# Kernel tuning notes

Hardware: AMD Instinct MI355X
Metric: run time of the kernel (lower is better)

## Reference

```python
import jax, jax.numpy as jnp
import numpy as np

B, C, S, E, H = 16, 24, 128, 256, 8
P = E // H  # head projection dim (consistent interpretation of the buggy source)
EPS = 1e-6


def _ln(x, g, b):
    mu = jnp.mean(x, axis=-1, keepdims=True)
    var = jnp.mean((x - mu) ** 2, axis=-1, keepdims=True)
    return (x - mu) * jax.lax.rsqrt(var + EPS) * g + b


def setup_inputs() -> dict:
    key = jax.random.key(0)
    ks = jax.random.split(key, 16)
    s = 0.02
    return {
        'x': jax.random.normal(ks[0], (B, C, S, E), jnp.float32),
        # spatial attention params
        'Wq_s': s * jax.random.normal(ks[1], (H, C, P, E), jnp.float32),
        'Wk_s': s * jax.random.normal(ks[2], (H, E, P), jnp.float32),
        'Wv_s': s * jax.random.normal(ks[3], (H, E, P), jnp.float32),
        'Wo_s': s * jax.random.normal(ks[4], (C, E, E), jnp.float32),
        # temporal attention params
        'Wq_t': s * jax.random.normal(ks[5], (H, C, E, P), jnp.float32),
        'Wk_t': s * jax.random.normal(ks[6], (H, C, E, P), jnp.float32),
        'Wv_t': s * jax.random.normal(ks[7], (H, C, E, P), jnp.float32),
        'Wo_t': s * jax.random.normal(ks[8], (C, E, E), jnp.float32),
        # shared layernorm
        'ln_g': jnp.ones((E,), jnp.float32),
        'ln_b': jnp.zeros((E,), jnp.float32),
        # per-joint pointwise FF (Linear->ReLU->Linear)
        'ff_w1': s * jax.random.normal(ks[9], (C, E, E), jnp.float32),
        'ff_b1': jnp.zeros((C, E), jnp.float32),
        'ff_w2': s * jax.random.normal(ks[10], (C, E, E), jnp.float32),
        'ff_b2': jnp.zeros((C, E), jnp.float32),
    }


def _spatial_attention(x, Wq, Wk, Wv, Wo):
    # x: [B,C,S,E]; per-head per-joint query proj, shared key/value proj
    q = jnp.einsum('bcse,hcpe->bshcp', x, Wq)          # [B,S,H,C,P]
    k = jnp.einsum('bcse,hep->bshcp', x, Wk)
    v = jnp.einsum('bcse,hep->bshcp', x, Wv)
    scores = jnp.einsum('bshcp,bshdp->bshcd', q, k) / jnp.sqrt(jnp.float32(P))
    a = jax.nn.softmax(scores, axis=-1)                # attn over joints d
    o = jnp.einsum('bshcd,bshdp->bshcp', a, v)
    o = o.transpose(0, 3, 1, 2, 4).reshape(x.shape[0], C, x.shape[2], H * P)  # [B,C,S,E]
    return jnp.einsum('bcse,cef->bcsf', o, Wo)


def _temporal_attention(x, Wq, Wk, Wv, Wo):
    q = jnp.einsum('bcse,hcep->bhcsp', x, Wq)          # [B,H,C,S,P]
    k = jnp.einsum('bcse,hcep->bhcsp', x, Wk)
    v = jnp.einsum('bcse,hcep->bhcsp', x, Wv)
    scores = jnp.einsum('bhcsp,bhctp->bhcst', q, k) / jnp.sqrt(jnp.float32(P))
    a = jax.nn.softmax(scores, axis=-1)                # attn over time t
    o = jnp.einsum('bhcst,bhctp->bhcsp', a, v)
    o = o.transpose(0, 2, 3, 1, 4).reshape(x.shape[0], C, x.shape[2], H * P)  # [B,C,S,E]
    return jnp.einsum('bcse,cef->bcsf', o, Wo)


def reference(x, Wq_s, Wk_s, Wv_s, Wo_s, Wq_t, Wk_t, Wv_t, Wo_t, ln_g, ln_b, ff_w1, ff_b1, ff_w2, ff_b2):
    spat = _spatial_attention(x, Wq_s, Wk_s, Wv_s, Wo_s)
    temp = _temporal_attention(x, Wq_t, Wk_t, Wv_t, Wo_t)
    attn_out = _ln(x + spat, ln_g, ln_b) + _ln(x + temp, ln_g, ln_b)
    # per-joint pointwise FF, vectorized over joints
    h = jax.nn.relu(jnp.einsum('bcse,cef->bcsf', attn_out, ff_w1) + ff_b1[None, :, None, :])
    ff = jnp.einsum('bcse,cef->bcsf', h, ff_w2) + ff_b2[None, :, None, :]
    return _ln(attn_out + ff, ln_g, ln_b)
```

## Files before the change

### kernel.cpp

```cpp
#include <hip/hip_runtime.h>
#include <hip/hip_bf16.h>

constexpr int Bn = 16, Cn = 24, Sn = 128, En = 256, Hn = 8, Pn = 32;
constexpr int NROWS = Bn * Cn * Sn;
constexpr size_t NBUF = (size_t)Bn * Cn * Sn * En;
constexpr size_t WSLOT = (size_t)Cn * 256 * 256;

typedef __bf16 bf16_t;
typedef bf16_t bf16x8 __attribute__((ext_vector_type(8)));
typedef bf16_t bf16x4 __attribute__((ext_vector_type(4)));
typedef float f32x4 __attribute__((ext_vector_type(4)));

__device__ __forceinline__ void gl2lds16(const bf16_t* g, bf16_t* l) {
    typedef const __attribute__((address_space(1))) unsigned int* gp_t;
    typedef __attribute__((address_space(3))) unsigned int* lp_t;
    __builtin_amdgcn_global_load_lds((gp_t)(unsigned long long)g,
                                     (lp_t)(unsigned int)(unsigned long long)l,
                                     16, 0, 0);
}

__global__ __launch_bounds__(256) void conv_x_k(const float* __restrict__ x,
                                                bf16_t* __restrict__ xb) {
    const size_t i = ((size_t)blockIdx.x * 256 + threadIdx.x) * 4;
    const float4 v = *(const float4*)(x + i);
    bf16x4 o = {(bf16_t)v.x, (bf16_t)v.y, (bf16_t)v.z, (bf16_t)v.w};
    *(bf16x4*)(xb + i) = o;
}

__global__ __launch_bounds__(256) void conv_w_copy_k(const float* __restrict__ W,
                                                     bf16_t* __restrict__ out) {
    const int row = blockIdx.x * 4 + (threadIdx.x >> 6);
    const int lane = threadIdx.x & 63;
    const int n = row & 255, c = row >> 8;
    const float* src = W + (size_t)c * (Pn * En) + (size_t)(n >> 5) * (Cn * Pn * En) +
                       (size_t)(n & 31) * En + lane * 4;
    const float4 v = *(const float4*)src;
    bf16x4 o = {(bf16_t)v.x, (bf16_t)v.y, (bf16_t)v.z, (bf16_t)v.w};
    *(bf16x4*)(out + (size_t)row * 256 + lane * 4) = o;
}

struct TDesc { const float* W; int Sc, Snh, Se; };

__global__ __launch_bounds__(256) void conv_w_tr_k(
    TDesc d0, TDesc d1, TDesc d2, TDesc d3, TDesc d4, TDesc d5, TDesc d6,
    bf16_t* __restrict__ out)
{
    TDesc d;
    switch (blockIdx.z) {
        case 0: d = d0; break; case 1: d = d1; break; case 2: d = d2; break;
        case 3: d = d3; break; case 4: d = d4; break; case 5: d = d5; break;
        default: d = d6; break;
    }
    const int g = blockIdx.x & 7, et = blockIdx.x >> 3;
    const int c = blockIdx.y;

    __shared__ float tile[32][65];

    const int t = threadIdx.x;
    const float* base = d.W + (size_t)c * d.Sc + (size_t)g * d.Snh;

#pragma unroll
    for (int pass = 0; pass < 2; ++pass) {
        const int e_local = pass * 32 + (t >> 3);
        const int j4 = (t & 7) * 4;
        const float4 v = *(const float4*)(base + (size_t)(et * 64 + e_local) * d.Se + j4);
        tile[j4 + 0][e_local] = v.x;
        tile[j4 + 1][e_local] = v.y;
        tile[j4 + 2][e_local] = v.z;
        tile[j4 + 3][e_local] = v.w;
    }
    __syncthreads();

    const int j = t >> 3, e8 = (t & 7) * 8;
    bf16x8 o;
#pragma unroll
    for (int k = 0; k < 8; ++k) o[k] = (bf16_t)tile[j][e8 + k];
    *(bf16x8*)(out + (size_t)blockIdx.z * WSLOT +
               ((size_t)c * 256 + g * 32 + j) * 256 + et * 64 + e8) = o;
}

__global__ __launch_bounds__(256) void conv_w_k(const float* __restrict__ W,
                                                bf16_t* __restrict__ Wb,
                                                int Sc, int Snh, int Snp, int Se) {
    const int n = blockIdx.x & 255, c = blockIdx.x >> 8;
    const int e = threadIdx.x;
    Wb[(size_t)blockIdx.x * 256 + e] =
        (bf16_t)W[(size_t)c * Sc + (size_t)(n >> 5) * Snh + (n & 31) * Snp + (size_t)e * Se];
}

struct GDesc { const bf16_t* W; bf16_t* O; int Aoff, Wc, Ob, Oc, Os, Onh, Onp, trans; };

template <int NP, int EPI>
__global__ __launch_bounds__(256) void gemm_mfma(
    const bf16_t* __restrict__ A, int Ab, int Ac, int As,
    GDesc g0, GDesc g1, GDesc g2, const float* __restrict__ bias)
{
    const int b = blockIdx.x, c = blockIdx.z;
    const int proj = (NP == 1) ? 0 : ((int)blockIdx.y >> 1);
    const int nt = (NP == 1) ? (int)blockIdx.y : ((int)blockIdx.y & 1);
    GDesc g = (proj == 0) ? g0 : (proj == 1) ? g1 : g2;

    __shared__ bf16_t smem[3][2][128 * 32];
    bf16_t* Cs = &smem[0][0][0];

    const int tid = threadIdx.x, wv = tid >> 6, ln = tid & 63;
    const int wm = (wv >> 1) * 64, wn = (wv & 1) * 64;
    const int lr = ln & 15, hi = ln >> 4, lk = hi * 8;

    const bf16_t* Abase = A + g.Aoff + (size_t)b * Ab + (size_t)c * Ac;
    const bf16_t* Bbase = g.W + (size_t)c * g.Wc + (size_t)(nt * 128) * 256;

    auto stage = [&](int buf, int kt) {
        const int k0 = kt * 32;
#pragma unroll
        for (int it = 0; it < 2; ++it) {
            const int cb = it * 256 + wv * 64;
            const int mc = cb + ln;
            const int row = mc >> 2, kc = (mc & 3) * 8;
            gl2lds16(Abase + (size_t)row * As + k0 + kc, &smem[buf][0][cb * 8]);
            gl2lds16(Bbase + (size_t)row * 256 + k0 + kc, &smem[buf][1][cb * 8]);
        }
    };

    f32x4 acc[4][4] = {};

    stage(0, 0);
    stage(1, 1);

#pragma unroll
    for (int kt = 0; kt < 8; ++kt) {
        if (kt < 6) stage((kt + 2) % 3, kt + 2);
        if (kt < 6)       asm volatile("s_waitcnt vmcnt(8)" ::: "memory");
        else if (kt == 6) asm volatile("s_waitcnt vmcnt(4)" ::: "memory");
        else              asm volatile("s_waitcnt vmcnt(0)" ::: "memory");
        __builtin_amdgcn_s_barrier();
        __builtin_amdgcn_sched_barrier(0);

        const int cur = kt % 3;
        bf16x8 af[4], bfr[4];
#pragma unroll
        for (int i = 0; i < 4; ++i)
            af[i] = *(const bf16x8*)&smem[cur][0][(wm + i * 16 + lr) * 32 + lk];
#pragma unroll
        for (int j = 0; j < 4; ++j)
            bfr[j] = *(const bf16x8*)&smem[cur][1][(wn + j * 16 + lr) * 32 + lk];
        __builtin_amdgcn_s_setprio(1);
#pragma unroll
        for (int i = 0; i < 4; ++i)
#pragma unroll
            for (int j = 0; j < 4; ++j)
                acc[i][j] = __builtin_amdgcn_mfma_f32_16x16x32_bf16(af[i], bfr[j], acc[i][j], 0, 0, 0);
        __builtin_amdgcn_s_setprio(0);

        __builtin_amdgcn_sched_barrier(0);
        __builtin_amdgcn_s_barrier();
    }

#pragma unroll
    for (int pass = 0; pass < 2; ++pass) {
        if (!g.trans) {
            if (wm == pass * 64) {
#pragma unroll
                for (int i = 0; i < 4; ++i)
#pragma unroll
                    for (int j = 0; j < 4; ++j) {
                        const int n = nt * 128 + wn + j * 16 + lr;
                        float bv = 0.f;
                        if (EPI) bv = bias[c * 256 + n];
#pragma unroll
                        for (int r = 0; r < 4; ++r) {
                            float v = acc[i][j][r];
                            if (EPI) { v += bv; if (EPI == 1) v = fmaxf(v, 0.f); }
                            Cs[(i * 16 + hi * 4 + r) * 136 + wn + j * 16 + lr] = (bf16_t)v;
                        }
                    }
            }
            __syncthreads();
#pragma unroll
            for (int it = 0; it < 2; ++it) {
                const int lrow = it * 32 + (tid >> 3);
                const int n0 = (tid & 7) * 16;
                bf16x8 v0 = *(const bf16x8*)&Cs[lrow * 136 + n0];
                bf16x8 v1 = *(const bf16x8*)&Cs[lrow * 136 + n0 + 8];
                const int m = pass * 64 + lrow;
                const int n = nt * 128 + n0;
                bf16_t* dst = g.O + (size_t)b * g.Ob + (size_t)c * g.Oc +
                              (size_t)m * g.Os + (size_t)(n >> 5) * g.Onh + (n & 31);
                *(bf16x8*)dst = v0;
                *(bf16x8*)(dst + 8) = v1;
            }
            __syncthreads();
        } else {
            if (wn == pass * 64) {
#pragma unroll
                for (int i = 0; i < 4; ++i)
#pragma unroll
                    for (int j = 0; j < 4; ++j) {
                        bf16x4 pk = {(bf16_t)acc[i][j][0], (bf16_t)acc[i][j][1],
                                     (bf16_t)acc[i][j][2], (bf16_t)acc[i][j][3]};
                        *(bf16x4*)&Cs[(j * 16 + lr) * 136 + wm + i * 16 + hi * 4] = pk;
                    }
            }
            __syncthreads();
#pragma unroll
            for (int it = 0; it < 2; ++it) {
                const int lrow = it * 32 + (tid >> 3);
                const int m0 = (tid & 7) * 16;
                bf16x8 v0 = *(const bf16x8*)&Cs[lrow * 136 + m0];
                bf16x8 v1 = *(const bf16x8*)&Cs[lrow * 136 + m0 + 8];
                const int n = nt * 128 + pass * 64 + lrow;
                bf16_t* dst = g.O + (size_t)b * g.Ob + (size_t)c * g.Oc +
                              (size_t)(n >> 5) * g.Onh + (size_t)(n & 31) * g.Onp + m0;
                *(bf16x8*)dst = v0;
                *(bf16x8*)(dst + 8) = v1;
            }
            __syncthreads();
        }
    }
}

__global__ __launch_bounds__(256) void attn_spatial_mfma(
    const bf16_t* __restrict__ Q, const bf16_t* __restrict__ K,
    const bf16_t* __restrict__ V, bf16_t* __restrict__ O)
{
    __shared__ bf16_t Ps[4][32 * 40];
    __shared__ bf16_t Vt[4][32 * 40];

    const int tid = threadIdx.x, wv = tid >> 6, ln = tid & 63;
    const int lr = ln & 15, hi = ln >> 4, lk = hi * 8;

    const int bsh = blockIdx.x * 4 + wv;
    const int h = bsh & 7, s = (bsh >> 3) & 127, b = bsh >> 10;
    const size_t qb = (size_t)bsh * (Cn * Pn);

    {
        const int p = ln >> 1, c0 = 24 + (ln & 1) * 4;
        bf16x4 z = {};
        *(bf16x4*)&Vt[wv][p * 40 + c0] = z;
    }
#pragma unroll
    for (int it = 0; it < 2; ++it) {
        const int ch = it * 64 + ln;
        if (ch < 96) {
            const int cc = ch >> 2, p0 = (ch & 3) * 8;
            bf16x8 v = *(const bf16x8*)(V + qb + cc * 32 + p0);
#pragma unroll
            for (int j = 0; j < 8; ++j)
                Vt[wv][(p0 + j) * 40 + cc] = v[j];
        }
    }

    bf16x8 aq0 = *(const bf16x8*)(Q + qb + lr * 32 + lk);
    bf16x8 aq1 = *(const bf16x8*)(Q + qb + (16 + lr) * 32 + lk);
    bf16x8 bk0 = *(const bf16x8*)(K + qb + lr * 32 + lk);
    bf16x8 bk1 = *(const bf16x8*)(K + qb + (16 + lr) * 32 + lk);
    const f32x4 zz = {0.f, 0.f, 0.f, 0.f};
    f32x4 sc[2][2];
    sc[0][0] = __builtin_amdgcn_mfma_f32_16x16x32_bf16(aq0, bk0, zz, 0, 0, 0);
    sc[0][1] = __builtin_amdgcn_mfma_f32_16x16x32_bf16(aq0, bk1, zz, 0, 0, 0);
    sc[1][0] = __builtin_amdgcn_mfma_f32_16x16x32_bf16(aq1, bk0, zz, 0, 0, 0);
    sc[1][1] = __builtin_amdgcn_mfma_f32_16x16x32_bf16(aq1, bk1, zz, 0, 0, 0);

    const float scale = 0.17677669529663687f;
#pragma unroll
    for (int i = 0; i < 2; ++i) {
        float s0[4], s1[4], mx[4];
#pragma unroll
        for (int r = 0; r < 4; ++r) {
            s0[r] = sc[i][0][r] * scale;
            s1[r] = (lr >= 8) ? -3.0e38f : sc[i][1][r] * scale;
            mx[r] = fmaxf(s0[r], s1[r]);
        }
#pragma unroll
        for (int d = 1; d < 16; d <<= 1)
#pragma unroll
            for (int r = 0; r < 4; ++r) mx[r] = fmaxf(mx[r], __shfl_xor(mx[r], d));
        float e0[4], e1[4], sm[4];
#pragma unroll
        for (int r = 0; r < 4; ++r) {
            e0[r] = __expf(s0[r] - mx[r]);
            e1[r] = __expf(s1[r] - mx[r]);
            sm[r] = e0[r] + e1[r];
        }
#pragma unroll
        for (int d = 1; d < 16; d <<= 1)
#pragma unroll
            for (int r = 0; r < 4; ++r) sm[r] += __shfl_xor(sm[r], d);
#pragma unroll
        for (int r = 0; r < 4; ++r) {
            const float inv = 1.f / sm[r];
            const int row = i * 16 + hi * 4 + r;
            Ps[wv][row * 40 + lr]      = (bf16_t)(e0[r] * inv);
            Ps[wv][row * 40 + 16 + lr] = (bf16_t)(e1[r] * inv);
        }
    }

    bf16x8 ap0 = *(const bf16x8*)&Ps[wv][lr * 40 + lk];
    bf16x8 ap1 = *(const bf16x8*)&Ps[wv][(16 + lr) * 40 + lk];
    bf16x8 bv0 = *(const bf16x8*)&Vt[wv][lr * 40 + lk];
    bf16x8 bv1 = *(const bf16x8*)&Vt[wv][(16 + lr) * 40 + lk];
    f32x4 o[2][2];
    o[0][0] = __builtin_amdgcn_mfma_f32_16x16x32_bf16(ap0, bv0, zz, 0, 0, 0);
    o[0][1] = __builtin_amdgcn_mfma_f32_16x16x32_bf16(ap0, bv1, zz, 0, 0, 0);
    o[1][0] = __builtin_amdgcn_mfma_f32_16x16x32_bf16(ap1, bv0, zz, 0, 0, 0);
    o[1][1] = __builtin_amdgcn_mfma_f32_16x16x32_bf16(ap1, bv1, zz, 0, 0, 0);

#pragma unroll
    for (int i = 0; i < 2; ++i)
#pragma unroll
        for (int r = 0; r < 4; ++r) {
            const int c = i * 16 + hi * 4 + r;
            if (c < 24) {
                const size_t ob = ((size_t)(b * Cn + c) * Sn + s) * En + h * Pn;
#pragma unroll
                for (int j = 0; j < 2; ++j)
                    O[ob + j * 16 + lr] = (bf16_t)o[i][j][r];
            }
        }
}

__global__ __launch_bounds__(256) void attn_temporal_mfma(
    const bf16_t* __restrict__ Q, const bf16_t* __restrict__ K,
    const bf16_t* __restrict__ Vt, bf16_t* __restrict__ O)
{
    const int c = blockIdx.x, h = blockIdx.y, b = blockIdx.z;
    const size_t base = ((size_t)(b * Hn + h) * Cn + c) * (Sn * Pn);

    __shared__ bf16_t Qs[128 * 32];
    __shared__ bf16_t Ks[128 * 32];
    __shared__ bf16_t Vs[32 * 136];
    __shared__ bf16_t Ps[128 * 136];

    const int tid = threadIdx.x, wv = tid >> 6, ln = tid & 63;
    const int lr = ln & 15, lk = (ln >> 4) * 8;

#pragma unroll
    for (int it = 0; it < 2; ++it) {
        const int cb = it * 256 + wv * 64;
        const int mc = cb + ln;
        const int row = mc >> 2, kc = (mc & 3) * 8;
        gl2lds16(Q + base + row * 32 + kc, &Qs[cb * 8]);
        gl2lds16(K + base + row * 32 + kc, &Ks[cb * 8]);
    }
#pragma unroll
    for (int it = 0; it < 2; ++it) {
        const int mc = it * 256 + tid;
        const int p = mc >> 4, scn = (mc & 15) * 8;
        bf16x8 v = *(const bf16x8*)(Vt + base + p * 128 + scn);
        *(bf16x8*)&Vs[p * 136 + scn] = v;
    }
    __syncthreads();

    const int r0 = wv * 32;
    bf16x8 aq0 = *(const bf16x8*)&Qs[(r0 + lr) * 32 + lk];
    bf16x8 aq1 = *(const bf16x8*)&Qs[(r0 + 16 + lr) * 32 + lk];
    f32x4 sc_[2][8];
    const f32x4 zz = {0.f, 0.f, 0.f, 0.f};
#pragma unroll
    for (int j = 0; j < 8; ++j) {
        bf16x8 bk = *(const bf16x8*)&Ks[(j * 16 + lr) * 32 + lk];
        sc_[0][j] = __builtin_amdgcn_mfma_f32_16x16x32_bf16(aq0, bk, zz, 0, 0, 0);
        sc_[1][j] = __builtin_amdgcn_mfma_f32_16x16x32_bf16(aq1, bk, zz, 0, 0, 0);
    }

    const float scale = 0.17677669529663687f;
#pragma unroll
    for (int i = 0; i < 2; ++i) {
        float mx[4], sm[4];
#pragma unroll
        for (int r = 0; r < 4; ++r) {
            float m = sc_[i][0][r];
#pragma unroll
            for (int j = 1; j < 8; ++j) m = fmaxf(m, sc_[i][j][r]);
            mx[r] = m;
        }
#pragma unroll
        for (int d = 1; d < 16; d <<= 1)
#pragma unroll
            for (int r = 0; r < 4; ++r) mx[r] = fmaxf(mx[r], __shfl_xor(mx[r], d));
#pragma unroll
        for (int r = 0; r < 4; ++r) sm[r] = 0.f;
#pragma unroll
        for (int j = 0; j < 8; ++j)
#pragma unroll
            for (int r = 0; r < 4; ++r) {
                const float e = __expf((sc_[i][j][r] - mx[r]) * scale);
                sc_[i][j][r] = e; sm[r] += e;
            }
#pragma unroll
        for (int d = 1; d < 16; d <<= 1)
#pragma unroll
            for (int r = 0; r < 4; ++r) sm[r] += __shfl_xor(sm[r], d);
        float inv[4];
#pragma unroll
        for (int r = 0; r < 4; ++r) inv[r] = 1.f / sm[r];
        const int rb = r0 + i * 16 + (ln >> 4) * 4;
#pragma unroll
        for (int j = 0; j < 8; ++j)
#pragma unroll
            for (int r = 0; r < 4; ++r)
                Ps[(rb + r) * 136 + j * 16 + lr] = (bf16_t)(sc_[i][j][r] * inv[r]);
    }
    __syncthreads();

    f32x4 o[2][2] = {};
#pragma unroll
    for (int kk = 0; kk < 4; ++kk) {
        bf16x8 ap0 = *(const bf16x8*)&Ps[(r0 + lr) * 136 + kk * 32 + lk];
        bf16x8 ap1 = *(const bf16x8*)&Ps[(r0 + 16 + lr) * 136 + kk * 32 + lk];
        bf16x8 bv0 = *(const bf16x8*)&Vs[lr * 136 + kk * 32 + lk];
        bf16x8 bv1 = *(const bf16x8*)&Vs[(16 + lr) * 136 + kk * 32 + lk];
        o[0][0] = __builtin_amdgcn_mfma_f32_16x16x32_bf16(ap0, bv0, o[0][0], 0, 0, 0);
        o[0][1] = __builtin_amdgcn_mfma_f32_16x16x32_bf16(ap0, bv1, o[0][1], 0, 0, 0);
        o[1][0] = __builtin_amdgcn_mfma_f32_16x16x32_bf16(ap1, bv0, o[1][0], 0, 0, 0);
        o[1][1] = __builtin_amdgcn_mfma_f32_16x16x32_bf16(ap1, bv1, o[1][1], 0, 0, 0);
    }

#pragma unroll
    for (int i = 0; i < 2; ++i) {
        const int sb = r0 + i * 16 + (ln >> 4) * 4;
#pragma unroll
        for (int j = 0; j < 2; ++j) {
            const int p = h * 32 + j * 16 + lr;
#pragma unroll
            for (int r = 0; r < 4; ++r)
                O[((size_t)(b * Cn + c) * Sn + (sb + r)) * En + p] = (bf16_t)o[i][j][r];
        }
    }
}

__global__ __launch_bounds__(256) void ln_combine_k(
    const bf16_t* __restrict__ xb, const bf16_t* __restrict__ spat,
    const bf16_t* __restrict__ temp, const float* __restrict__ g,
    const float* __restrict__ beta, bf16_t* __restrict__ AO)
{
    const int row = blockIdx.x * 4 + (threadIdx.x >> 6);
    const int lane = threadIdx.x & 63;
    const size_t off = (size_t)row * En;

    float v1[4], v2[4];
    float s1 = 0, s2 = 0, q1 = 0, q2 = 0;
#pragma unroll
    for (int i = 0; i < 4; i++) {
        const int e = lane + i * 64;
        const float xv = (float)xb[off + e];
        const float a = xv + (float)spat[off + e];
        const float t = xv + (float)temp[off + e];
        v1[i] = a; v2[i] = t;
        s1 += a; s2 += t; q1 += a * a; q2 += t * t;
    }
    for (int d = 32; d; d >>= 1) {
        s1 += __shfl_xor(s1, d); s2 += __shfl_xor(s2, d);
        q1 += __shfl_xor(q1, d); q2 += __shfl_xor(q2, d);
    }
    const float mu1 = s1 / En, mu2 = s2 / En;
    const float r1 = rsqrtf(q1 / En - mu1 * mu1 + 1e-6f);
    const float r2 = rsqrtf(q2 / En - mu2 * mu2 + 1e-6f);
#pragma unroll
    for (int i = 0; i < 4; i++) {
        const int e = lane + i * 64;
        const float out = (v1[i] - mu1) * r1 * g[e] + beta[e] +
                          (v2[i] - mu2) * r2 * g[e] + beta[e];
        AO[off + e] = (bf16_t)out;
    }
}

__global__ __launch_bounds__(256) void ln_final_k(
    const bf16_t* __restrict__ AO, const bf16_t* __restrict__ FF,
    const float* __restrict__ g, const float* __restrict__ beta,
    float* __restrict__ out)
{
    const int row = blockIdx.x * 4 + (threadIdx.x >> 6);
    const int lane = threadIdx.x & 63;
    const size_t off = (size_t)row * En;

    float v[4];
    float s = 0, q = 0;
#pragma unroll
    for (int i = 0; i < 4; i++) {
        const int e = lane + i * 64;
        const float a = (float)AO[off + e] + (float)FF[off + e];
        v[i] = a; s += a; q += a * a;
    }
    for (int d = 32; d; d >>= 1) { s += __shfl_xor(s, d); q += __shfl_xor(q, d); }
    const float mu = s / En;
    const float r = rsqrtf(q / En - mu * mu + 1e-6f);
#pragma unroll
    for (int i = 0; i < 4; i++) {
        const int e = lane + i * 64;
        out[off + e] = (v[i] - mu) * r * g[e] + beta[e];
    }
}

extern "C" void kernel_launch(void* const* d_in, const int* in_sizes, int n_in,
                              void* d_out, int out_size, void* d_ws, size_t ws_size,
                              hipStream_t stream)
{
    const float* x     = (const float*)d_in[0];
    const float* Wq_s  = (const float*)d_in[1];
    const float* Wk_s  = (const float*)d_in[2];
    const float* Wv_s  = (const float*)d_in[3];
    const float* Wo_s  = (const float*)d_in[4];
    const float* Wq_t  = (const float*)d_in[5];
    const float* Wk_t  = (const float*)d_in[6];
    const float* Wv_t  = (const float*)d_in[7];
    const float* Wo_t  = (const float*)d_in[8];
    const float* ln_g  = (const float*)d_in[9];
    const float* ln_b  = (const float*)d_in[10];
    const float* ff_w1 = (const float*)d_in[11];
    const float* ff_b1 = (const float*)d_in[12];
    const float* ff_w2 = (const float*)d_in[13];
    const float* ff_b2 = (const float*)d_in[14];
    float* out = (float*)d_out;

    bf16_t* wsb = (bf16_t*)d_ws;
    bf16_t* b0 = wsb;
    bf16_t* b1 = wsb + NBUF;
    bf16_t* b2 = wsb + 2 * NBUF;
    bf16_t* b3 = wsb + 3 * NBUF;
    bf16_t* b4 = wsb + 4 * NBUF;

    bf16_t* xb = (bf16_t*)d_out;
    bf16_t* wb = xb + NBUF;
    bf16_t* w_qs = wb + 0 * WSLOT;
    bf16_t* wtr  = wb + 1 * WSLOT;
    bf16_t* w_os = wtr + 0 * WSLOT;
    bf16_t* w_qt = wtr + 1 * WSLOT;
    bf16_t* w_kt = wtr + 2 * WSLOT;
    bf16_t* w_vt = wtr + 3 * WSLOT;
    bf16_t* w_ot = wtr + 4 * WSLOT;
    bf16_t* w_f1 = wtr + 5 * WSLOT;
    bf16_t* w_f2 = wtr + 6 * WSLOT;
    bf16_t* w_ks = b4 + NBUF - 2 * 65536;
    bf16_t* w_vs = b4 + NBUF - 65536;

    const int XAb = Cn * Sn * En, XAc = Sn * En, XAs = En;
    const int QSb = Sn * Hn * Cn * Pn, QSs = Hn * Cn * Pn, QSh = Cn * Pn;
    const int QTb = Hn * Cn * Sn * Pn, QTh = Cn * Sn * Pn, QTc = Sn * Pn, QTs = Pn;
    const int WCP = 256 * 256;

    conv_x_k<<<NBUF / 1024, 256, 0, stream>>>(x, xb);
    conv_w_copy_k<<<1536, 256, 0, stream>>>(Wq_s, w_qs);
    conv_w_tr_k<<<dim3(32, 24, 7), 256, 0, stream>>>(
        TDesc{Wo_s, En * En, Pn, En},
        TDesc{Wq_t, En * Pn, Cn * En * Pn, Pn},
        TDesc{Wk_t, En * Pn, Cn * En * Pn, Pn},
        TDesc{Wv_t, En * Pn, Cn * En * Pn, Pn},
        TDesc{Wo_t, En * En, Pn, En},
        TDesc{ff_w1, En * En, Pn, En},
        TDesc{ff_w2, En * En, Pn, En},
        wtr);
    conv_w_k<<<256, 256, 0, stream>>>(Wk_s, w_ks, 0, En * Pn, 1, Pn);
    conv_w_k<<<256, 256, 0, stream>>>(Wv_s, w_vs, 0, En * Pn, 1, Pn);

    gemm_mfma<3, 0><<<dim3(16, 6, 24), 256, 0, stream>>>(
        xb, XAb, XAc, XAs,
        GDesc{w_qs, b0, 0, WCP, QSb, Pn, QSs, QSh, 1, 0},
        GDesc{w_ks, b1, 0, 0,   QSb, Pn, QSs, QSh, 1, 0},
        GDesc{w_vs, b2, 0, 0,   QSb, Pn, QSs, QSh, 1, 0},
        nullptr);
    attn_spatial_mfma<<<Bn * Sn * Hn / 4, 256, 0, stream>>>(b0, b1, b2, b3);

    gemm_mfma<3, 0><<<dim3(16, 6, 24), 256, 0, stream>>>(
        xb, XAb, XAc, XAs,
        GDesc{w_qt, b0, 0, WCP, QTb, QTc, QTs, QTh, 1, 0},
        GDesc{w_kt, b1, 0, WCP, QTb, QTc, QTs, QTh, 1, 0},
        GDesc{w_vt, b2, 0, WCP, QTb, QTc, 1, QTh, Sn, 1},
        nullptr);
    attn_temporal_mfma<<<dim3(24, 8, 16), 256, 0, stream>>>(b0, b1, b2, b4);

    gemm_mfma<2, 0><<<dim3(16, 4, 24), 256, 0, stream>>>(
        b3, XAb, XAc, XAs,
        GDesc{w_os, b0, 0,          WCP, XAb, XAc, XAs, 32, 1, 0},
        GDesc{w_ot, b1, (int)NBUF,  WCP, XAb, XAc, XAs, 32, 1, 0},
        GDesc{w_os, b0, 0,          WCP, XAb, XAc, XAs, 32, 1, 0}, nullptr);

    ln_combine_k<<<NROWS / 4, 256, 0, stream>>>(xb, b0, b1, ln_g, ln_b, b2);
    gemm_mfma<1, 1><<<dim3(16, 2, 24), 256, 0, stream>>>(
        b2, XAb, XAc, XAs,
        GDesc{w_f1, b3, 0, WCP, XAb, XAc, XAs, 32, 1, 0},
        GDesc{w_f1, b3, 0, WCP, XAb, XAc, XAs, 32, 1, 0},
        GDesc{w_f1, b3, 0, WCP, XAb, XAc, XAs, 32, 1, 0}, ff_b1);
    gemm_mfma<1, 2><<<dim3(16, 2, 24), 256, 0, stream>>>(
        b3, XAb, XAc, XAs,
        GDesc{w_f2, b4, 0, WCP, XAb, XAc, XAs, 32, 1, 0},
        GDesc{w_f2, b4, 0, WCP, XAb, XAc, XAs, 32, 1, 0},
        GDesc{w_f2, b4, 0, WCP, XAb, XAc, XAs, 32, 1, 0}, ff_b2);
    ln_final_k<<<NROWS / 4, 256, 0, stream>>>(b2, b4, ln_g, ln_b, out);
}
```

Measured before the change: 387.8 us.

## Enlarge GEMM tile to 256x128 spanning two batches per block

```diff
diff --git a/kernel.cpp b/kernel.cpp
--- a/kernel.cpp
+++ b/kernel.cpp
@@ -91,38 +91,43 @@
 struct GDesc { const bf16_t* W; bf16_t* O; int Aoff, Wc, Ob, Oc, Os, Onh, Onp, trans; };
 
 template <int NP, int EPI>
-__global__ __launch_bounds__(256) void gemm_mfma(
+__global__ __launch_bounds__(256, 2) void gemm_mfma(
     const bf16_t* __restrict__ A, int Ab, int Ac, int As,
     GDesc g0, GDesc g1, GDesc g2, const float* __restrict__ bias)
 {
-    const int b = blockIdx.x, c = blockIdx.z;
+    const int bx = blockIdx.x, c = blockIdx.z;
     const int proj = (NP == 1) ? 0 : ((int)blockIdx.y >> 1);
     const int nt = (NP == 1) ? (int)blockIdx.y : ((int)blockIdx.y & 1);
     GDesc g = (proj == 0) ? g0 : (proj == 1) ? g1 : g2;
 
-    __shared__ bf16_t smem[3][2][128 * 32];
-    bf16_t* Cs = &smem[0][0][0];
+    __shared__ bf16_t smem[3][12288];
+    bf16_t* Cs = &smem[0][0];
 
     const int tid = threadIdx.x, wv = tid >> 6, ln = tid & 63;
-    const int wm = (wv >> 1) * 64, wn = (wv & 1) * 64;
+    const int wm = wv * 64;
     const int lr = ln & 15, hi = ln >> 4, lk = hi * 8;
 
-    const bf16_t* Abase = A + g.Aoff + (size_t)b * Ab + (size_t)c * Ac;
+    const bf16_t* Abase = A + g.Aoff + (size_t)(bx * 2) * Ab + (size_t)c * Ac;
     const bf16_t* Bbase = g.W + (size_t)c * g.Wc + (size_t)(nt * 128) * 256;
 
     auto stage = [&](int buf, int kt) {
         const int k0 = kt * 32;
 #pragma unroll
-        for (int it = 0; it < 2; ++it) {
-            const int cb = it * 256 + wv * 64;
-            const int mc = cb + ln;
-            const int row = mc >> 2, kc = (mc & 3) * 8;
-            gl2lds16(Abase + (size_t)row * As + k0 + kc, &smem[buf][0][cb * 8]);
-            gl2lds16(Bbase + (size_t)row * 256 + k0 + kc, &smem[buf][1][cb * 8]);
+        for (int ga = 0; ga < 4; ++ga) {
+            const int ch = ga * 256 + wv * 64 + ln;
+            const int row = ch >> 2, q = (ch & 3) * 8;
+            gl2lds16(Abase + (size_t)(row >> 7) * Ab + (size_t)(row & 127) * As + k0 + q,
+                     &smem[buf][ch * 8]);
+        }
+#pragma unroll
+        for (int gb = 0; gb < 2; ++gb) {
+            const int ch = gb * 256 + wv * 64 + ln;
+            const int row = ch >> 2, q = (ch & 3) * 8;
+            gl2lds16(Bbase + (size_t)row * 256 + k0 + q, &smem[buf][8192 + ch * 8]);
         }
     };
 
-    f32x4 acc[4][4] = {};
+    f32x4 acc[4][8] = {};
 
     stage(0, 0);
     stage(1, 1);
@@ -130,26 +135,25 @@
 #pragma unroll
     for (int kt = 0; kt < 8; ++kt) {
         if (kt < 6) stage((kt + 2) % 3, kt + 2);
-        if (kt < 6)       asm volatile("s_waitcnt vmcnt(8)" ::: "memory");
-        else if (kt == 6) asm volatile("s_waitcnt vmcnt(4)" ::: "memory");
+        if (kt < 6)       asm volatile("s_waitcnt vmcnt(12)" ::: "memory");
+        else if (kt == 6) asm volatile("s_waitcnt vmcnt(6)" ::: "memory");
         else              asm volatile("s_waitcnt vmcnt(0)" ::: "memory");
         __builtin_amdgcn_s_barrier();
         __builtin_amdgcn_sched_barrier(0);
 
         const int cur = kt % 3;
-        bf16x8 af[4], bfr[4];
+        bf16x8 af[4];
 #pragma unroll
         for (int i = 0; i < 4; ++i)
-            af[i] = *(const bf16x8*)&smem[cur][0][(wm + i * 16 + lr) * 32 + lk];
-#pragma unroll
-        for (int j = 0; j < 4; ++j)
-            bfr[j] = *(const bf16x8*)&smem[cur][1][(wn + j * 16 + lr) * 32 + lk];
+            af[i] = *(const bf16x8*)&smem[cur][(wm + i * 16 + lr) * 32 + lk];
         __builtin_amdgcn_s_setprio(1);
 #pragma unroll
-        for (int i = 0; i < 4; ++i)
-#pragma unroll
-            for (int j = 0; j < 4; ++j)
-                acc[i][j] = __builtin_amdgcn_mfma_f32_16x16x32_bf16(af[i], bfr[j], acc[i][j], 0, 0, 0);
+        for (int j = 0; j < 8; ++j) {
+            bf16x8 bf = *(const bf16x8*)&smem[cur][8192 + (j * 16 + lr) * 32 + lk];
+#pragma unroll
+            for (int i = 0; i < 4; ++i)
+                acc[i][j] = __builtin_amdgcn_mfma_f32_16x16x32_bf16(af[i], bf, acc[i][j], 0, 0, 0);
+        }
         __builtin_amdgcn_s_setprio(0);
 
         __builtin_amdgcn_sched_barrier(0);
@@ -159,58 +163,56 @@
 #pragma unroll
     for (int pass = 0; pass < 2; ++pass) {
         if (!g.trans) {
-            if (wm == pass * 64) {
+            if ((wv >> 1) == pass) {
 #pragma unroll
                 for (int i = 0; i < 4; ++i)
 #pragma unroll
-                    for (int j = 0; j < 4; ++j) {
-                        const int n = nt * 128 + wn + j * 16 + lr;
+                    for (int j = 0; j < 8; ++j) {
+                        const int n = nt * 128 + j * 16 + lr;
                         float bv = 0.f;
                         if (EPI) bv = bias[c * 256 + n];
 #pragma unroll
                         for (int r = 0; r < 4; ++r) {
                             float v = acc[i][j][r];
                             if (EPI) { v += bv; if (EPI == 1) v = fmaxf(v, 0.f); }
-                            Cs[(i * 16 + hi * 4 + r) * 136 + wn + j * 16 + lr] = (bf16_t)v;
+                            Cs[((wv & 1) * 64 + i * 16 + hi * 4 + r) * 136 + j * 16 + lr] = (bf16_t)v;
                         }
                     }
             }
             __syncthreads();
 #pragma unroll
-            for (int it = 0; it < 2; ++it) {
+            for (int it = 0; it < 4; ++it) {
                 const int lrow = it * 32 + (tid >> 3);
                 const int n0 = (tid & 7) * 16;
                 bf16x8 v0 = *(const bf16x8*)&Cs[lrow * 136 + n0];
                 bf16x8 v1 = *(const bf16x8*)&Cs[lrow * 136 + n0 + 8];
-                const int m = pass * 64 + lrow;
                 const int n = nt * 128 + n0;
-                bf16_t* dst = g.O + (size_t)b * g.Ob + (size_t)c * g.Oc +
-                              (size_t)m * g.Os + (size_t)(n >> 5) * g.Onh + (n & 31);
+                bf16_t* dst = g.O + (size_t)(bx * 2 + pass) * g.Ob + (size_t)c * g.Oc +
+                              (size_t)lrow * g.Os + (size_t)(n >> 5) * g.Onh + (n & 31);
                 *(bf16x8*)dst = v0;
                 *(bf16x8*)(dst + 8) = v1;
             }
             __syncthreads();
         } else {
-            if (wn == pass * 64) {
-#pragma unroll
-                for (int i = 0; i < 4; ++i)
-#pragma unroll
-                    for (int j = 0; j < 4; ++j) {
-                        bf16x4 pk = {(bf16_t)acc[i][j][0], (bf16_t)acc[i][j][1],
-                                     (bf16_t)acc[i][j][2], (bf16_t)acc[i][j][3]};
-                        *(bf16x4*)&Cs[(j * 16 + lr) * 136 + wm + i * 16 + hi * 4] = pk;
-                    }
-            }
+#pragma unroll
+            for (int i = 0; i < 4; ++i)
+#pragma unroll
+                for (int jj = 0; jj < 4; ++jj) {
+                    const int j = pass * 4 + jj;
+                    bf16x4 pk = {(bf16_t)acc[i][j][0], (bf16_t)acc[i][j][1],
+                                 (bf16_t)acc[i][j][2], (bf16_t)acc[i][j][3]};
+                    *(bf16x4*)&Cs[(jj * 16 + lr) * 264 + wm + i * 16 + hi * 4] = pk;
+                }
             __syncthreads();
 #pragma unroll
-            for (int it = 0; it < 2; ++it) {
-                const int lrow = it * 32 + (tid >> 3);
-                const int m0 = (tid & 7) * 16;
-                bf16x8 v0 = *(const bf16x8*)&Cs[lrow * 136 + m0];
-                bf16x8 v1 = *(const bf16x8*)&Cs[lrow * 136 + m0 + 8];
+            for (int it = 0; it < 4; ++it) {
+                const int lrow = it * 16 + (tid >> 4);
+                const int m0 = (tid & 15) * 16;
+                bf16x8 v0 = *(const bf16x8*)&Cs[lrow * 264 + m0];
+                bf16x8 v1 = *(const bf16x8*)&Cs[lrow * 264 + m0 + 8];
                 const int n = nt * 128 + pass * 64 + lrow;
-                bf16_t* dst = g.O + (size_t)b * g.Ob + (size_t)c * g.Oc +
-                              (size_t)(n >> 5) * g.Onh + (size_t)(n & 31) * g.Onp + m0;
+                bf16_t* dst = g.O + (size_t)(bx * 2 + (m0 >> 7)) * g.Ob + (size_t)c * g.Oc +
+                              (size_t)(n >> 5) * g.Onh + (size_t)(n & 31) * g.Onp + (m0 & 127);
                 *(bf16x8*)dst = v0;
                 *(bf16x8*)(dst + 8) = v1;
             }
@@ -553,7 +555,7 @@
     conv_w_k<<<256, 256, 0, stream>>>(Wk_s, w_ks, 0, En * Pn, 1, Pn);
     conv_w_k<<<256, 256, 0, stream>>>(Wv_s, w_vs, 0, En * Pn, 1, Pn);
 
-    gemm_mfma<3, 0><<<dim3(16, 6, 24), 256, 0, stream>>>(
+    gemm_mfma<3, 0><<<dim3(8, 6, 24), 256, 0, stream>>>(
         xb, XAb, XAc, XAs,
         GDesc{w_qs, b0, 0, WCP, QSb, Pn, QSs, QSh, 1, 0},
         GDesc{w_ks, b1, 0, 0,   QSb, Pn, QSs, QSh, 1, 0},
@@ -561,7 +563,7 @@
         nullptr);
     attn_spatial_mfma<<<Bn * Sn * Hn / 4, 256, 0, stream>>>(b0, b1, b2, b3);
 
-    gemm_mfma<3, 0><<<dim3(16, 6, 24), 256, 0, stream>>>(
+    gemm_mfma<3, 0><<<dim3(8, 6, 24), 256, 0, stream>>>(
         xb, XAb, XAc, XAs,
         GDesc{w_qt, b0, 0, WCP, QTb, QTc, QTs, QTh, 1, 0},
         GDesc{w_kt, b1, 0, WCP, QTb, QTc, QTs, QTh, 1, 0},
@@ -569,19 +571,19 @@
         nullptr);
     attn_temporal_mfma<<<dim3(24, 8, 16), 256, 0, stream>>>(b0, b1, b2, b4);
 
-    gemm_mfma<2, 0><<<dim3(16, 4, 24), 256, 0, stream>>>(
+    gemm_mfma<2, 0><<<dim3(8, 4, 24), 256, 0, stream>>>(
         b3, XAb, XAc, XAs,
         GDesc{w_os, b0, 0,          WCP, XAb, XAc, XAs, 32, 1, 0},
         GDesc{w_ot, b1, (int)NBUF,  WCP, XAb, XAc, XAs, 32, 1, 0},
         GDesc{w_os, b0, 0,          WCP, XAb, XAc, XAs, 32, 1, 0}, nullptr);
 
     ln_combine_k<<<NROWS / 4, 256, 0, stream>>>(xb, b0, b1, ln_g, ln_b, b2);
-    gemm_mfma<1, 1><<<dim3(16, 2, 24), 256, 0, stream>>>(
+    gemm_mfma<1, 1><<<dim3(8, 2, 24), 256, 0, stream>>>(
         b2, XAb, XAc, XAs,
         GDesc{w_f1, b3, 0, WCP, XAb, XAc, XAs, 32, 1, 0},
         GDesc{w_f1, b3, 0, WCP, XAb, XAc, XAs, 32, 1, 0},
         GDesc{w_f1, b3, 0, WCP, XAb, XAc, XAs, 32, 1, 0}, ff_b1);
-    gemm_mfma<1, 2><<<dim3(16, 2, 24), 256, 0, stream>>>(
+    gemm_mfma<1, 2><<<dim3(8, 2, 24), 256, 0, stream>>>(
         b3, XAb, XAc, XAs,
         GDesc{w_f2, b4, 0, WCP, XAb, XAc, XAs, 32, 1, 0},
         GDesc{w_f2, b4, 0, WCP, XAb, XAc, XAs, 32, 1, 0},
```

Measured after the change: 399.9 us. +3.1%, slower.
